# Kernel tuning notes

Measured on AMD Instinct MI355X. Metric: run time of the kernel, lower is better.

The kernel has to match this reference:

```python
import jax, jax.numpy as jnp
from jax import lax
import numpy as np

STRIDE = 8  # == slice_width
EMBED_DIM = 512


def setup_inputs() -> dict:
    key = jax.random.key(0)
    k0, k1, k2, k3, k4 = jax.random.split(key, 5)
    B, C, H, W = 64, 1, 32, 8192
    images = jax.random.normal(k0, (B, C, H, W), dtype=jnp.float32)
    u = lambda k, s: jax.random.uniform(k, s, jnp.float32, -0.08, 0.08)
    conv_w = u(k1, (1, 1, 3, 3))            # OIHW, 1->1 channel, 3x3
    conv_b = u(k2, (1,))
    lin_w = u(k3, (H * STRIDE, EMBED_DIM))   # bridge: slice_height*slice_width -> embed_dim
    lin_b = u(k4, (EMBED_DIM,))
    return {"images": images, "conv_w": conv_w, "conv_b": conv_b, "lin_w": lin_w, "lin_b": lin_b}


def reference(images, conv_w, conv_b, lin_w, lin_b):
    B, C, H, W = images.shape
    S = W // STRIDE  # src_len (number of width-slices)
    # Windowing: non-overlapping width slices -> a single reshape/transpose
    # [B, C, H, W] -> [B*S, C, H, stride]
    sl = images.reshape(B, C, H, S, STRIDE).transpose(0, 3, 1, 2, 4)
    pixels = sl.reshape(B * S, C, H, STRIDE)
    # Conv2d(1,1,3x3, padding=1) + ReLU (same spatial shape)
    y = lax.conv_general_dilated(
        pixels, conv_w, window_strides=(1, 1), padding="SAME",
        dimension_numbers=("NCHW", "OIHW", "NCHW"))
    y = jax.nn.relu(y + conv_b[None, :, None, None])
    # Bridge linear on flattened slice pixels
    feats = y.reshape(B * S, H * STRIDE)
    emb = feats @ lin_w + lin_b
    return emb.reshape(B, S, EMBED_DIM)
```

## Files before the change

### kernel.cpp

```cpp
#include <hip/hip_runtime.h>
#include <hip/hip_bf16.h>
#include <stdint.h>

#define HEIGHT 32
#define WIDTH  8192
#define KDIM   256
#define NDIM   512
#define NSLICES 65536
#define NMTILES (NSLICES / 32)
#define WT_BYTES (NDIM * KDIM * 2)

typedef float f32x4  __attribute__((ext_vector_type(4)));
typedef float f32x16 __attribute__((ext_vector_type(16)));
typedef short bf16x8 __attribute__((ext_vector_type(8)));

__device__ __forceinline__ ushort f2bf(float x) {
  union { float f; uint32_t u; } un; un.f = x;
  uint32_t u = un.u;
  u += 0x7FFFu + ((u >> 16) & 1u);
  return (ushort)(u >> 16);
}

__device__ __forceinline__ void load_row8(float* r, const float* p) {
  f32x4 lo = *reinterpret_cast<const f32x4*>(p);
  f32x4 hi = *reinterpret_cast<const f32x4*>(p + 4);
#pragma unroll
  for (int w = 0; w < 4; ++w) { r[w] = lo[w]; r[4 + w] = hi[w]; }
}

__global__ __launch_bounds__(256) void prep_wt2_kernel(const float* __restrict__ lin_w,
                                                       ushort* __restrict__ wt2) {
  const int idx = blockIdx.x * 256 + threadIdx.x;
  const int ln  = idx & 63;
  const int k0  = (idx >> 6) & 15;
  const int nb  = idx >> 10;
  const int n   = nb * 32 + (ln & 31);
  const int kb  = k0 * 16 + (ln >> 5) * 8;
  bf16x8 p;
#pragma unroll
  for (int e = 0; e < 8; ++e) p[e] = (short)f2bf(lin_w[(size_t)(kb + e) * NDIM + n]);
  *reinterpret_cast<bf16x8*>(wt2 + (size_t)idx * 8) = p;
}

__global__ __launch_bounds__(256) void fused_kernel(
    const float* __restrict__ images, const float* __restrict__ conv_w,
    const float* __restrict__ conv_b, const ushort* __restrict__ wt2,
    const float* __restrict__ lin_b, float* __restrict__ out) {
  __shared__ ushort A[16 * 64 * 8];

  const int tid  = threadIdx.x;
  const int blk  = blockIdx.x;

  float cw[9];
#pragma unroll
  for (int i = 0; i < 9; ++i) cw[i] = conv_w[i];
  const float cb = conv_b[0];

  {
    const int sl = tid & 31;
    const int q  = tid >> 5;
    const int s  = blk * 32 + sl;
    const int b  = s >> 10;
    const int slb = s & 1023;
    const float* base = images + (size_t)b * (HEIGHT * WIDTH) + (size_t)slb * 8;
    const int h0 = q * 4;

    float r[6][8];
#pragma unroll
    for (int i = 0; i < 6; ++i) {
      const int h = h0 - 1 + i;
      if (h >= 0 && h < HEIGHT) load_row8(r[i], base + (size_t)h * WIDTH);
      else {
#pragma unroll
        for (int w = 0; w < 8; ++w) r[i][w] = 0.f;
      }
    }

#pragma unroll
    for (int oh = 0; oh < 4; ++oh) {
      const int h = h0 + oh;
      float y[8];
#pragma unroll
      for (int w = 0; w < 8; ++w) y[w] = cb;
#pragma unroll
      for (int dh = 0; dh < 3; ++dh) {
#pragma unroll
        for (int dw = 0; dw < 3; ++dw) {
          const float c = cw[dh * 3 + dw];
#pragma unroll
          for (int w = 0; w < 8; ++w) {
            const int iw = w + dw - 1;
            if (iw >= 0 && iw < 8) y[w] = fmaf(r[oh + dh][iw], c, y[w]);
          }
        }
      }
      bf16x8 pack;
#pragma unroll
      for (int w = 0; w < 8; ++w) pack[w] = (short)f2bf(fmaxf(y[w], 0.f));
      const int ln = ((h & 1) << 5) | sl;
      const int k0 = h >> 1;
      *reinterpret_cast<bf16x8*>(A + ((size_t)k0 * 64 + ln) * 8) = pack;
    }
  }
  __syncthreads();

  const int lane = tid & 63;
  const int wv   = tid >> 6;
  const int la   = lane & 31;
  const int lb   = lane >> 5;

  const ushort* abase = A + (size_t)lane * 8;
  const ushort* bbase = wt2 + ((size_t)(wv * 4) * 16) * 512 + (size_t)lane * 8;

  f32x16 acc[4];
#pragma unroll
  for (int nf = 0; nf < 4; ++nf)
#pragma unroll
    for (int i = 0; i < 16; ++i) acc[nf][i] = 0.f;

#pragma unroll
  for (int k0 = 0; k0 < 16; ++k0) {
    const bf16x8 af = *reinterpret_cast<const bf16x8*>(abase + (size_t)k0 * 512);
    bf16x8 bfr[4];
#pragma unroll
    for (int nf = 0; nf < 4; ++nf)
      bfr[nf] = *reinterpret_cast<const bf16x8*>(bbase + (size_t)(nf * 16 + k0) * 512);
#pragma unroll
    for (int nf = 0; nf < 4; ++nf)
      acc[nf] = __builtin_amdgcn_mfma_f32_32x32x16_bf16(af, bfr[nf], acc[nf], 0, 0, 0);
  }

  const size_t row0 = (size_t)blk * 32;
#pragma unroll
  for (int nf = 0; nf < 4; ++nf) {
    const int col = wv * 128 + nf * 32 + la;
    const float bias = lin_b[col];
#pragma unroll
    for (int reg = 0; reg < 16; ++reg) {
      const int rr = (reg & 3) + 8 * (reg >> 2) + 4 * lb;
      out[(row0 + rr) * NDIM + col] = acc[nf][reg] + bias;
    }
  }
}

extern "C" void kernel_launch(void* const* d_in, const int* in_sizes, int n_in,
                              void* d_out, int out_size, void* d_ws, size_t ws_size,
                              hipStream_t stream) {
  const float* images = (const float*)d_in[0];
  const float* conv_w = (const float*)d_in[1];
  const float* conv_b = (const float*)d_in[2];
  const float* lin_w  = (const float*)d_in[3];
  const float* lin_b  = (const float*)d_in[4];
  float* out = (float*)d_out;
  ushort* wt2 = (ushort*)d_ws;

  hipLaunchKernelGGL(prep_wt2_kernel, dim3(64), dim3(256), 0, stream, lin_w, wt2);
  hipLaunchKernelGGL(fused_kernel, dim3(NMTILES), dim3(256), 0, stream,
                     images, conv_w, conv_b, wt2, lin_b, out);
}
```

Baseline: 54.22 us.

## Double block M-tile to 64 slices with 2x2 MFMA register blocking

Each block now handles 64 slices instead of 32, so the weight fragments read from global memory are reused across two M fragments, halving B traffic per output. The conv stage gives each thread 8 rows of one slice using a rolling three-row window, which reduces redundant halo row loads. The GEMM is split into two passes of 2x2 accumulator tiles to keep register pressure similar. LDS use doubles and the grid halves, which may lower occupancy and parallelism.

```diff
diff --git a/kernel.cpp b/kernel.cpp
--- a/kernel.cpp
+++ b/kernel.cpp
@@ -7,8 +7,8 @@
 #define KDIM   256
 #define NDIM   512
 #define NSLICES 65536
-#define NMTILES (NSLICES / 32)
-#define WT_BYTES (NDIM * KDIM * 2)
+#define BM     64
+#define NBLOCKS (NSLICES / BM)
 
 typedef float f32x4  __attribute__((ext_vector_type(4)));
 typedef float f32x16 __attribute__((ext_vector_type(16)));
@@ -46,10 +46,10 @@
     const float* __restrict__ images, const float* __restrict__ conv_w,
     const float* __restrict__ conv_b, const ushort* __restrict__ wt2,
     const float* __restrict__ lin_b, float* __restrict__ out) {
-  __shared__ ushort A[16 * 64 * 8];
+  __shared__ ushort A[2 * 16 * 64 * 8];
 
-  const int tid  = threadIdx.x;
-  const int blk  = blockIdx.x;
+  const int tid = threadIdx.x;
+  const int blk = blockIdx.x;
 
   float cw[9];
 #pragma unroll
@@ -57,49 +57,56 @@
   const float cb = conv_b[0];
 
   {
-    const int sl = tid & 31;
-    const int q  = tid >> 5;
-    const int s  = blk * 32 + sl;
+    const int sl = tid & 63;
+    const int q  = tid >> 6;
+    const int s  = blk * 64 + sl;
     const int b  = s >> 10;
     const int slb = s & 1023;
     const float* base = images + (size_t)b * (HEIGHT * WIDTH) + (size_t)slb * 8;
-    const int h0 = q * 4;
+    const int h0 = q * 8;
+    const int mf = sl >> 5;
+    const int la = sl & 31;
 
-    float r[6][8];
+    float pr[8], cu[8], nx[8];
+    if (h0 > 0) load_row8(pr, base + (size_t)(h0 - 1) * WIDTH);
+    else {
 #pragma unroll
-    for (int i = 0; i < 6; ++i) {
-      const int h = h0 - 1 + i;
-      if (h >= 0 && h < HEIGHT) load_row8(r[i], base + (size_t)h * WIDTH);
+      for (int w = 0; w < 8; ++w) pr[w] = 0.f;
+    }
+    load_row8(cu, base + (size_t)h0 * WIDTH);
+
+#pragma unroll
+    for (int i = 0; i < 8; ++i) {
+      const int h = h0 + i;
+      if (h + 1 < HEIGHT) load_row8(nx, base + (size_t)(h + 1) * WIDTH);
       else {
 #pragma unroll
-        for (int w = 0; w < 8; ++w) r[i][w] = 0.f;
+        for (int w = 0; w < 8; ++w) nx[w] = 0.f;
       }
-    }
-
-#pragma unroll
-    for (int oh = 0; oh < 4; ++oh) {
-      const int h = h0 + oh;
       float y[8];
 #pragma unroll
       for (int w = 0; w < 8; ++w) y[w] = cb;
 #pragma unroll
-      for (int dh = 0; dh < 3; ++dh) {
+      for (int dw = 0; dw < 3; ++dw) {
+        const float c0 = cw[dw], c1 = cw[3 + dw], c2 = cw[6 + dw];
 #pragma unroll
-        for (int dw = 0; dw < 3; ++dw) {
-          const float c = cw[dh * 3 + dw];
-#pragma unroll
-          for (int w = 0; w < 8; ++w) {
-            const int iw = w + dw - 1;
-            if (iw >= 0 && iw < 8) y[w] = fmaf(r[oh + dh][iw], c, y[w]);
+        for (int w = 0; w < 8; ++w) {
+          const int iw = w + dw - 1;
+          if (iw >= 0 && iw < 8) {
+            y[w] = fmaf(pr[iw], c0, y[w]);
+            y[w] = fmaf(cu[iw], c1, y[w]);
+            y[w] = fmaf(nx[iw], c2, y[w]);
           }
         }
       }
       bf16x8 pack;
 #pragma unroll
       for (int w = 0; w < 8; ++w) pack[w] = (short)f2bf(fmaxf(y[w], 0.f));
-      const int ln = ((h & 1) << 5) | sl;
       const int k0 = h >> 1;
-      *reinterpret_cast<bf16x8*>(A + ((size_t)k0 * 64 + ln) * 8) = pack;
+      const int ln = ((h & 1) << 5) | la;
+      *reinterpret_cast<bf16x8*>(A + (((size_t)mf * 16 + k0) * 64 + ln) * 8) = pack;
+#pragma unroll
+      for (int w = 0; w < 8; ++w) { pr[w] = cu[w]; cu[w] = nx[w]; }
     }
   }
   __syncthreads();
@@ -108,37 +115,48 @@
   const int wv   = tid >> 6;
   const int la   = lane & 31;
   const int lb   = lane >> 5;
+  const size_t row0 = (size_t)blk * BM;
 
-  const ushort* abase = A + (size_t)lane * 8;
-  const ushort* bbase = wt2 + ((size_t)(wv * 4) * 16) * 512 + (size_t)lane * 8;
-
-  f32x16 acc[4];
-#pragma unroll
-  for (int nf = 0; nf < 4; ++nf)
-#pragma unroll
-    for (int i = 0; i < 16; ++i) acc[nf][i] = 0.f;
+  const ushort* a0 = A + (size_t)lane * 8;
+  const ushort* a1 = A + (size_t)(16 * 64 + lane) * 8;
 
 #pragma unroll
-  for (int k0 = 0; k0 < 16; ++k0) {
-    const bf16x8 af = *reinterpret_cast<const bf16x8*>(abase + (size_t)k0 * 512);
-    bf16x8 bfr[4];
+  for (int pass = 0; pass < 2; ++pass) {
+    const int nfb = wv * 4 + pass * 2;
+    const ushort* bb = wt2 + ((size_t)nfb * 16) * 512 + (size_t)lane * 8;
+
+    f32x16 acc[2][2];
 #pragma unroll
-    for (int nf = 0; nf < 4; ++nf)
-      bfr[nf] = *reinterpret_cast<const bf16x8*>(bbase + (size_t)(nf * 16 + k0) * 512);
+    for (int mf = 0; mf < 2; ++mf)
 #pragma unroll
-    for (int nf = 0; nf < 4; ++nf)
-      acc[nf] = __builtin_amdgcn_mfma_f32_32x32x16_bf16(af, bfr[nf], acc[nf], 0, 0, 0);
-  }
+      for (int nf = 0; nf < 2; ++nf)
+#pragma unroll
+        for (int i = 0; i < 16; ++i) acc[mf][nf][i] = 0.f;
 
-  const size_t row0 = (size_t)blk * 32;
 #pragma unroll
-  for (int nf = 0; nf < 4; ++nf) {
-    const int col = wv * 128 + nf * 32 + la;
-    const float bias = lin_b[col];
+    for (int k0 = 0; k0 < 16; ++k0) {
+      const bf16x8 af0 = *reinterpret_cast<const bf16x8*>(a0 + (size_t)k0 * 512);
+      const bf16x8 af1 = *reinterpret_cast<const bf16x8*>(a1 + (size_t)k0 * 512);
+      const bf16x8 bf0 = *reinterpret_cast<const bf16x8*>(bb + (size_t)k0 * 512);
+      const bf16x8 bf1 = *reinterpret_cast<const bf16x8*>(bb + (size_t)(16 + k0) * 512);
+      acc[0][0] = __builtin_amdgcn_mfma_f32_32x32x16_bf16(af0, bf0, acc[0][0], 0, 0, 0);
+      acc[1][0] = __builtin_amdgcn_mfma_f32_32x32x16_bf16(af1, bf0, acc[1][0], 0, 0, 0);
+      acc[0][1] = __builtin_amdgcn_mfma_f32_32x32x16_bf16(af0, bf1, acc[0][1], 0, 0, 0);
+      acc[1][1] = __builtin_amdgcn_mfma_f32_32x32x16_bf16(af1, bf1, acc[1][1], 0, 0, 0);
+    }
+
 #pragma unroll
-    for (int reg = 0; reg < 16; ++reg) {
-      const int rr = (reg & 3) + 8 * (reg >> 2) + 4 * lb;
-      out[(row0 + rr) * NDIM + col] = acc[nf][reg] + bias;
+    for (int mf = 0; mf < 2; ++mf) {
+#pragma unroll
+      for (int nf = 0; nf < 2; ++nf) {
+        const int col = (nfb + nf) * 32 + la;
+        const float bias = lin_b[col];
+#pragma unroll
+        for (int reg = 0; reg < 16; ++reg) {
+          const int rr = mf * 32 + (reg & 3) + 8 * (reg >> 2) + 4 * lb;
+          out[(row0 + rr) * NDIM + col] = acc[mf][nf][reg] + bias;
+        }
+      }
     }
   }
 }
@@ -155,6 +173,6 @@
   ushort* wt2 = (ushort*)d_ws;
 
   hipLaunchKernelGGL(prep_wt2_kernel, dim3(64), dim3(256), 0, stream, lin_w, wt2);
-  hipLaunchKernelGGL(fused_kernel, dim3(NMTILES), dim3(256), 0, stream,
+  hipLaunchKernelGGL(fused_kernel, dim3(NBLOCKS), dim3(256), 0, stream,
                      images, conv_w, conv_b, wt2, lin_b, out);
 }
```

Result: slower. 56.99 us (+5.1%).

## Warp-specialize fused kernel into producer conv and consumer MFMA groups with double buffering

Applied to the files above, without the earlier changes.

The fused kernel now runs 512 threads per block, each block handling four 32-slice tiles. One 256-thread group computes conv+ReLU into one of two LDS buffers while the other group runs the MFMA GEMM and output stores for the previous tile, with a barrier between stages. The consumer splits its N range into two passes of two fragments to cut accumulator registers and raises wave priority around the MFMAs. The aim is to overlap image loads and conv math with matrix work and output writes. The cost is fewer blocks in the grid, half the threads idle at each pipeline end, and a serial per-block pipeline that may limit latency hiding compared with many independent blocks.

```diff
diff --git a/kernel.cpp b/kernel.cpp
--- a/kernel.cpp
+++ b/kernel.cpp
@@ -7,8 +7,9 @@
 #define KDIM   256
 #define NDIM   512
 #define NSLICES 65536
-#define NMTILES (NSLICES / 32)
-#define WT_BYTES (NDIM * KDIM * 2)
+#define BM     32
+#define TTILES 4
+#define NBLOCKS (NSLICES / (BM * TTILES))
 
 typedef float f32x4  __attribute__((ext_vector_type(4)));
 typedef float f32x16 __attribute__((ext_vector_type(16)));
@@ -42,104 +43,121 @@
   *reinterpret_cast<bf16x8*>(wt2 + (size_t)idx * 8) = p;
 }
 
-__global__ __launch_bounds__(256) void fused_kernel(
+__global__ __launch_bounds__(512) void fused_kernel(
     const float* __restrict__ images, const float* __restrict__ conv_w,
     const float* __restrict__ conv_b, const ushort* __restrict__ wt2,
     const float* __restrict__ lin_b, float* __restrict__ out) {
-  __shared__ ushort A[16 * 64 * 8];
+  __shared__ ushort A[2][16 * 64 * 8];
 
-  const int tid  = threadIdx.x;
-  const int blk  = blockIdx.x;
+  const int tid = threadIdx.x;
+  const int grp = tid >> 8;
+  const int blk = blockIdx.x;
 
   float cw[9];
 #pragma unroll
   for (int i = 0; i < 9; ++i) cw[i] = conv_w[i];
   const float cb = conv_b[0];
 
-  {
-    const int sl = tid & 31;
-    const int q  = tid >> 5;
-    const int s  = blk * 32 + sl;
-    const int b  = s >> 10;
-    const int slb = s & 1023;
-    const float* base = images + (size_t)b * (HEIGHT * WIDTH) + (size_t)slb * 8;
-    const int h0 = q * 4;
+  const int c_sl = tid & 31;
+  const int c_q  = (tid >> 5) & 7;
+  const int c_h0 = c_q * 4;
 
-    float r[6][8];
-#pragma unroll
-    for (int i = 0; i < 6; ++i) {
-      const int h = h0 - 1 + i;
-      if (h >= 0 && h < HEIGHT) load_row8(r[i], base + (size_t)h * WIDTH);
-      else {
-#pragma unroll
-        for (int w = 0; w < 8; ++w) r[i][w] = 0.f;
-      }
-    }
+  const int gt   = tid & 255;
+  const int lane = gt & 63;
+  const int wv   = gt >> 6;
+  const int la   = lane & 31;
+  const int lb   = lane >> 5;
 
 #pragma unroll
-    for (int oh = 0; oh < 4; ++oh) {
-      const int h = h0 + oh;
-      float y[8];
+  for (int s = 0; s <= TTILES; ++s) {
+    if (grp == 0) {
+      if (s < TTILES) {
+        const int t   = blk * TTILES + s;
+        const int gsl = t * BM + c_sl;
+        const int b   = gsl >> 10;
+        const int slb = gsl & 1023;
+        const float* base = images + (size_t)b * (HEIGHT * WIDTH) + (size_t)slb * 8;
+        ushort* Ab = A[s & 1];
+
+        float r[6][8];
 #pragma unroll
-      for (int w = 0; w < 8; ++w) y[w] = cb;
+        for (int i = 0; i < 6; ++i) {
+          const int h = c_h0 - 1 + i;
+          if (h >= 0 && h < HEIGHT) load_row8(r[i], base + (size_t)h * WIDTH);
+          else {
 #pragma unroll
-      for (int dh = 0; dh < 3; ++dh) {
+            for (int w = 0; w < 8; ++w) r[i][w] = 0.f;
+          }
+        }
+
 #pragma unroll
-        for (int dw = 0; dw < 3; ++dw) {
-          const float c = cw[dh * 3 + dw];
+        for (int oh = 0; oh < 4; ++oh) {
+          const int h = c_h0 + oh;
+          float y[8];
 #pragma unroll
-          for (int w = 0; w < 8; ++w) {
-            const int iw = w + dw - 1;
-            if (iw >= 0 && iw < 8) y[w] = fmaf(r[oh + dh][iw], c, y[w]);
+          for (int w = 0; w < 8; ++w) y[w] = cb;
+#pragma unroll
+          for (int dh = 0; dh < 3; ++dh) {
+#pragma unroll
+            for (int dw = 0; dw < 3; ++dw) {
+              const float c = cw[dh * 3 + dw];
+#pragma unroll
+              for (int w = 0; w < 8; ++w) {
+                const int iw = w + dw - 1;
+                if (iw >= 0 && iw < 8) y[w] = fmaf(r[oh + dh][iw], c, y[w]);
+              }
+            }
+          }
+          bf16x8 pack;
+#pragma unroll
+          for (int w = 0; w < 8; ++w) pack[w] = (short)f2bf(fmaxf(y[w], 0.f));
+          const int k0 = h >> 1;
+          const int ln = ((h & 1) << 5) | c_sl;
+          *reinterpret_cast<bf16x8*>(Ab + ((size_t)k0 * 64 + ln) * 8) = pack;
+        }
+      }
+    } else {
+      if (s >= 1) {
+        const int t = blk * TTILES + s - 1;
+        const ushort* abase = A[(s - 1) & 1] + (size_t)lane * 8;
+        const size_t row0 = (size_t)t * BM;
+
+#pragma unroll
+        for (int pass = 0; pass < 2; ++pass) {
+          const int nfb = wv * 4 + pass * 2;
+          const ushort* bb = wt2 + ((size_t)nfb * 16) * 512 + (size_t)lane * 8;
+
+          f32x16 acc[2];
+#pragma unroll
+          for (int nf = 0; nf < 2; ++nf)
+#pragma unroll
+            for (int i = 0; i < 16; ++i) acc[nf][i] = 0.f;
+
+#pragma unroll
+          for (int k0 = 0; k0 < 16; ++k0) {
+            const bf16x8 af  = *reinterpret_cast<const bf16x8*>(abase + (size_t)k0 * 512);
+            const bf16x8 bf0 = *reinterpret_cast<const bf16x8*>(bb + (size_t)k0 * 512);
+            const bf16x8 bf1 = *reinterpret_cast<const bf16x8*>(bb + (size_t)(16 + k0) * 512);
+            __builtin_amdgcn_s_setprio(1);
+            acc[0] = __builtin_amdgcn_mfma_f32_32x32x16_bf16(af, bf0, acc[0], 0, 0, 0);
+            acc[1] = __builtin_amdgcn_mfma_f32_32x32x16_bf16(af, bf1, acc[1], 0, 0, 0);
+            __builtin_amdgcn_s_setprio(0);
+          }
+
+#pragma unroll
+          for (int nf = 0; nf < 2; ++nf) {
+            const int col = (nfb + nf) * 32 + la;
+            const float bias = lin_b[col];
+#pragma unroll
+            for (int reg = 0; reg < 16; ++reg) {
+              const int rr = (reg & 3) + 8 * (reg >> 2) + 4 * lb;
+              out[(row0 + rr) * NDIM + col] = acc[nf][reg] + bias;
+            }
           }
         }
       }
-      bf16x8 pack;
-#pragma unroll
-      for (int w = 0; w < 8; ++w) pack[w] = (short)f2bf(fmaxf(y[w], 0.f));
-      const int ln = ((h & 1) << 5) | sl;
-      const int k0 = h >> 1;
-      *reinterpret_cast<bf16x8*>(A + ((size_t)k0 * 64 + ln) * 8) = pack;
     }
-  }
-  __syncthreads();
-
-  const int lane = tid & 63;
-  const int wv   = tid >> 6;
-  const int la   = lane & 31;
-  const int lb   = lane >> 5;
-
-  const ushort* abase = A + (size_t)lane * 8;
-  const ushort* bbase = wt2 + ((size_t)(wv * 4) * 16) * 512 + (size_t)lane * 8;
-
-  f32x16 acc[4];
-#pragma unroll
-  for (int nf = 0; nf < 4; ++nf)
-#pragma unroll
-    for (int i = 0; i < 16; ++i) acc[nf][i] = 0.f;
-
-#pragma unroll
-  for (int k0 = 0; k0 < 16; ++k0) {
-    const bf16x8 af = *reinterpret_cast<const bf16x8*>(abase + (size_t)k0 * 512);
-    bf16x8 bfr[4];
-#pragma unroll
-    for (int nf = 0; nf < 4; ++nf)
-      bfr[nf] = *reinterpret_cast<const bf16x8*>(bbase + (size_t)(nf * 16 + k0) * 512);
-#pragma unroll
-    for (int nf = 0; nf < 4; ++nf)
-      acc[nf] = __builtin_amdgcn_mfma_f32_32x32x16_bf16(af, bfr[nf], acc[nf], 0, 0, 0);
-  }
-
-  const size_t row0 = (size_t)blk * 32;
-#pragma unroll
-  for (int nf = 0; nf < 4; ++nf) {
-    const int col = wv * 128 + nf * 32 + la;
-    const float bias = lin_b[col];
-#pragma unroll
-    for (int reg = 0; reg < 16; ++reg) {
-      const int rr = (reg & 3) + 8 * (reg >> 2) + 4 * lb;
-      out[(row0 + rr) * NDIM + col] = acc[nf][reg] + bias;
-    }
+    __syncthreads();
   }
 }
 
@@ -155,6 +173,6 @@
   ushort* wt2 = (ushort*)d_ws;
 
   hipLaunchKernelGGL(prep_wt2_kernel, dim3(64), dim3(256), 0, stream, lin_w, wt2);
-  hipLaunchKernelGGL(fused_kernel, dim3(NMTILES), dim3(256), 0, stream,
+  hipLaunchKernelGGL(fused_kernel, dim3(NBLOCKS), dim3(512), 0, stream,
                      images, conv_w, conv_b, wt2, lin_b, out);
 }
```

Result: slower. 61.70 us (+13.8%).

## Compute conv A-fragments per wave in registers, removing LDS staging and barrier

Applied to the files above, without the earlier changes.

Each wave now computes its own conv+ReLU A-operand rows directly in registers, streaming image rows through a rolling three-row window across the K loop, and feeds them straight into the MFMAs. This removes the shared-memory tile, the block barrier and the LDS reads. The trade-off is that all four waves redundantly compute and load the same image data, quadrupling the conv work and the global image reads (these may hit in cache), and the loads are now interleaved with the MFMA chain.

```diff
diff --git a/kernel.cpp b/kernel.cpp
--- a/kernel.cpp
+++ b/kernel.cpp
@@ -7,8 +7,7 @@
 #define KDIM   256
 #define NDIM   512
 #define NSLICES 65536
-#define NMTILES (NSLICES / 32)
-#define WT_BYTES (NDIM * KDIM * 2)
+#define NMTILES 2048
 
 typedef float f32x4  __attribute__((ext_vector_type(4)));
 typedef float f32x16 __attribute__((ext_vector_type(16)));
@@ -42,74 +41,36 @@
   *reinterpret_cast<bf16x8*>(wt2 + (size_t)idx * 8) = p;
 }
 
-__global__ __launch_bounds__(256) void fused_kernel(
+__global__ __launch_bounds__(256) void fused_stream_kernel(
     const float* __restrict__ images, const float* __restrict__ conv_w,
     const float* __restrict__ conv_b, const ushort* __restrict__ wt2,
     const float* __restrict__ lin_b, float* __restrict__ out) {
-  __shared__ ushort A[16 * 64 * 8];
-
-  const int tid  = threadIdx.x;
-  const int blk  = blockIdx.x;
+  const int tid   = threadIdx.x;
+  const int lane  = tid & 63;
+  const int wv    = tid >> 6;
+  const int mtile = blockIdx.x;
+  const int sl    = lane & 31;
+  const int hi    = lane >> 5;
 
   float cw[9];
 #pragma unroll
   for (int i = 0; i < 9; ++i) cw[i] = conv_w[i];
   const float cb = conv_b[0];
 
-  {
-    const int sl = tid & 31;
-    const int q  = tid >> 5;
-    const int s  = blk * 32 + sl;
-    const int b  = s >> 10;
-    const int slb = s & 1023;
-    const float* base = images + (size_t)b * (HEIGHT * WIDTH) + (size_t)slb * 8;
-    const int h0 = q * 4;
+  const int s   = mtile * 32 + sl;
+  const int b   = s >> 10;
+  const int slb = s & 1023;
+  const float* base = images + (size_t)b * (HEIGHT * WIDTH) + (size_t)slb * 8;
 
-    float r[6][8];
+  float wa[8], wb[8], wc[8];
+  if (hi) load_row8(wa, base);
+  else {
 #pragma unroll
-    for (int i = 0; i < 6; ++i) {
-      const int h = h0 - 1 + i;
-      if (h >= 0 && h < HEIGHT) load_row8(r[i], base + (size_t)h * WIDTH);
-      else {
-#pragma unroll
-        for (int w = 0; w < 8; ++w) r[i][w] = 0.f;
-      }
-    }
+    for (int w = 0; w < 8; ++w) wa[w] = 0.f;
+  }
+  load_row8(wb, base + (size_t)hi * WIDTH);
+  load_row8(wc, base + (size_t)(hi + 1) * WIDTH);
 
-#pragma unroll
-    for (int oh = 0; oh < 4; ++oh) {
-      const int h = h0 + oh;
-      float y[8];
-#pragma unroll
-      for (int w = 0; w < 8; ++w) y[w] = cb;
-#pragma unroll
-      for (int dh = 0; dh < 3; ++dh) {
-#pragma unroll
-        for (int dw = 0; dw < 3; ++dw) {
-          const float c = cw[dh * 3 + dw];
-#pragma unroll
-          for (int w = 0; w < 8; ++w) {
-            const int iw = w + dw - 1;
-            if (iw >= 0 && iw < 8) y[w] = fmaf(r[oh + dh][iw], c, y[w]);
-          }
-        }
-      }
-      bf16x8 pack;
-#pragma unroll
-      for (int w = 0; w < 8; ++w) pack[w] = (short)f2bf(fmaxf(y[w], 0.f));
-      const int ln = ((h & 1) << 5) | sl;
-      const int k0 = h >> 1;
-      *reinterpret_cast<bf16x8*>(A + ((size_t)k0 * 64 + ln) * 8) = pack;
-    }
-  }
-  __syncthreads();
-
-  const int lane = tid & 63;
-  const int wv   = tid >> 6;
-  const int la   = lane & 31;
-  const int lb   = lane >> 5;
-
-  const ushort* abase = A + (size_t)lane * 8;
   const ushort* bbase = wt2 + ((size_t)(wv * 4) * 16) * 512 + (size_t)lane * 8;
 
   f32x16 acc[4];
@@ -120,24 +81,57 @@
 
 #pragma unroll
   for (int k0 = 0; k0 < 16; ++k0) {
-    const bf16x8 af = *reinterpret_cast<const bf16x8*>(abase + (size_t)k0 * 512);
-    bf16x8 bfr[4];
+    float y[8];
 #pragma unroll
-    for (int nf = 0; nf < 4; ++nf)
-      bfr[nf] = *reinterpret_cast<const bf16x8*>(bbase + (size_t)(nf * 16 + k0) * 512);
+    for (int w = 0; w < 8; ++w) y[w] = cb;
 #pragma unroll
-    for (int nf = 0; nf < 4; ++nf)
-      acc[nf] = __builtin_amdgcn_mfma_f32_32x32x16_bf16(af, bfr[nf], acc[nf], 0, 0, 0);
+    for (int dw = 0; dw < 3; ++dw) {
+      const float c0 = cw[dw], c1 = cw[3 + dw], c2 = cw[6 + dw];
+#pragma unroll
+      for (int w = 0; w < 8; ++w) {
+        const int iw = w + dw - 1;
+        if (iw >= 0 && iw < 8) {
+          y[w] = fmaf(wa[iw], c0, y[w]);
+          y[w] = fmaf(wb[iw], c1, y[w]);
+          y[w] = fmaf(wc[iw], c2, y[w]);
+        }
+      }
+    }
+    bf16x8 af;
+#pragma unroll
+    for (int w = 0; w < 8; ++w) af[w] = (short)f2bf(fmaxf(y[w], 0.f));
+
+    bf16x8 bf0 = *reinterpret_cast<const bf16x8*>(bbase + (size_t)k0 * 512);
+    bf16x8 bf1 = *reinterpret_cast<const bf16x8*>(bbase + (size_t)(16 + k0) * 512);
+    bf16x8 bf2 = *reinterpret_cast<const bf16x8*>(bbase + (size_t)(32 + k0) * 512);
+    bf16x8 bf3 = *reinterpret_cast<const bf16x8*>(bbase + (size_t)(48 + k0) * 512);
+    acc[0] = __builtin_amdgcn_mfma_f32_32x32x16_bf16(af, bf0, acc[0], 0, 0, 0);
+    acc[1] = __builtin_amdgcn_mfma_f32_32x32x16_bf16(af, bf1, acc[1], 0, 0, 0);
+    acc[2] = __builtin_amdgcn_mfma_f32_32x32x16_bf16(af, bf2, acc[2], 0, 0, 0);
+    acc[3] = __builtin_amdgcn_mfma_f32_32x32x16_bf16(af, bf3, acc[3], 0, 0, 0);
+
+    if (k0 < 15) {
+#pragma unroll
+      for (int w = 0; w < 8; ++w) wa[w] = wc[w];
+      const int rb_ = 2 * k0 + 2 + hi;
+      const int rc_ = 2 * k0 + 3 + hi;
+      load_row8(wb, base + (size_t)rb_ * WIDTH);
+      if (rc_ < HEIGHT) load_row8(wc, base + (size_t)rc_ * WIDTH);
+      else {
+#pragma unroll
+        for (int w = 0; w < 8; ++w) wc[w] = 0.f;
+      }
+    }
   }
 
-  const size_t row0 = (size_t)blk * 32;
+  const size_t row0 = (size_t)mtile * 32;
 #pragma unroll
   for (int nf = 0; nf < 4; ++nf) {
-    const int col = wv * 128 + nf * 32 + la;
+    const int col = wv * 128 + nf * 32 + sl;
     const float bias = lin_b[col];
 #pragma unroll
     for (int reg = 0; reg < 16; ++reg) {
-      const int rr = (reg & 3) + 8 * (reg >> 2) + 4 * lb;
+      const int rr = (reg & 3) + 8 * (reg >> 2) + 4 * hi;
       out[(row0 + rr) * NDIM + col] = acc[nf][reg] + bias;
     }
   }
@@ -155,6 +149,6 @@
   ushort* wt2 = (ushort*)d_ws;
 
   hipLaunchKernelGGL(prep_wt2_kernel, dim3(64), dim3(256), 0, stream, lin_w, wt2);
-  hipLaunchKernelGGL(fused_kernel, dim3(NMTILES), dim3(256), 0, stream,
+  hipLaunchKernelGGL(fused_stream_kernel, dim3(NMTILES), dim3(256), 0, stream,
                      images, conv_w, conv_b, wt2, lin_b, out);
 }
```

New measurement: 59.71 us. 10.1% more time.
